# Optimization experiments

Measured on AMD Instinct MI355X. Metric: run time of the kernel, lower is better.

## Reference

```python
import jax, jax.numpy as jnp
import numpy as np

POOL = 7  # cfg.POOLING_SIZE


def roi_align_avg(feat, rois, scale):
    """Legacy RoIAlignAvg: bilinearly sample a (POOL+1)x(POOL+1) grid per RoI
    (crop_and_resize semantics: grid spans roi with divisor G-1), then 2x2
    average-pool with stride 1 -> POOL x POOL output. feat: [B,C,H,W]."""
    B, C, H, W = feat.shape
    G = POOL + 1
    b = rois[:, 0].astype(jnp.int32)                                  # [R]
    x1 = rois[:, 1] * scale
    y1 = rois[:, 2] * scale
    x2 = rois[:, 3] * scale
    y2 = rois[:, 4] * scale
    t = jnp.arange(G, dtype=feat.dtype) / (G - 1)                     # [G]
    ty = jnp.clip(y1[:, None] + (y2 - y1)[:, None] * t, 0.0, H - 1)   # [R,G] rows
    tx = jnp.clip(x1[:, None] + (x2 - x1)[:, None] * t, 0.0, W - 1)   # [R,G] cols
    y0f, x0f = jnp.floor(ty), jnp.floor(tx)
    wy = (ty - y0f)[:, :, None, None]                                 # row frac
    wx = (tx - x0f)[:, None, :, None]                                 # col frac
    y0 = y0f.astype(jnp.int32)
    x0 = x0f.astype(jnp.int32)
    y1i = jnp.minimum(y0 + 1, H - 1)
    x1i = jnp.minimum(x0 + 1, W - 1)

    def g(yi, xi):  # point gather -> [R,G,G,C]
        return feat[b[:, None, None], :, yi[:, :, None], xi[:, None, :]]

    v = ((1 - wy) * ((1 - wx) * g(y0, x0) + wx * g(y0, x1i))
         + wy * ((1 - wx) * g(y1i, x0) + wx * g(y1i, x1i)))           # [R,G,G,C]
    v = jnp.transpose(v, (0, 3, 1, 2))                                # [R,C,G,G]
    # 2x2 avg pool, stride 1 -> [R,C,POOL,POOL]
    return 0.25 * (v[:, :, :-1, :-1] + v[:, :, 1:, :-1]
                   + v[:, :, :-1, 1:] + v[:, :, 1:, 1:])


def reference(p2, p3, p4, p5, rois, im_info):
    """_PyramidRoI_Feat (POOLING_MODE='align'): data-dependent FPN level
    assignment per RoI, per-level RoIAlignAvg, reassembled in original RoI
    order (equivalent to the concat+sort in the torch code)."""
    h = rois[:, 4] - rois[:, 2] + 1.0
    w = rois[:, 3] - rois[:, 1] + 1.0
    lvl = jnp.floor(jnp.log(jnp.sqrt(h * w) / 224.0) / np.float32(np.log(2.0)) + 4.0)
    lvl = jnp.clip(lvl, 2.0, 5.0)                                     # [R]
    im_h = im_info[0, 0]
    out = 0.0
    for l, feat in zip((2, 3, 4, 5), (p2, p3, p4, p5)):
        scale = feat.shape[2] / im_h
        mask = (lvl == l).astype(feat.dtype)[:, None, None, None]
        out = out + mask * roi_align_avg(feat, rois, scale)
    return out  # [R, C, POOL, POOL]


def setup_inputs() -> dict:
    key = jax.random.key(0)
    ks = jax.random.split(key, 6)
    B, C = 1, 256
    IMH = IMW = 1024.0
    R = 2000
    p2 = jax.random.normal(ks[0], (B, C, 256, 256), jnp.float32)
    p3 = jax.random.normal(ks[1], (B, C, 128, 128), jnp.float32)
    p4 = jax.random.normal(ks[2], (B, C, 64, 64), jnp.float32)
    p5 = jax.random.normal(ks[3], (B, C, 32, 32), jnp.float32)
    # log-uniform box sizes so RoIs spread across all 4 pyramid levels
    wh = jnp.exp(jax.random.uniform(ks[4], (R, 2), jnp.float32,
                                    minval=np.log(16.0), maxval=np.log(600.0)))
    xy = jax.random.uniform(ks[5], (R, 2), jnp.float32) * (jnp.array([IMW, IMH]) - wh)
    rois = jnp.concatenate([
        jnp.zeros((R, 1), jnp.float32),            # batch index
        xy[:, 0:1], xy[:, 1:2],                    # x1, y1
        xy[:, 0:1] + wh[:, 0:1] - 1.0,             # x2
        xy[:, 1:2] + wh[:, 1:2] - 1.0,             # y2
    ], axis=1)
    im_info = jnp.array([[IMH, IMW, 1.0]], jnp.float32)
    return {"p2": p2, "p3": p3, "p4": p4, "p5": p5, "rois": rois, "im_info": im_info}
```

## Files before the change

kernel.cpp:

```cpp
#include <hip/hip_runtime.h>
#include <hip/hip_fp16.h>
#include <math.h>

#define POOLSZ 7
#define GRIDG 8
#define CCH  256
#define NBIN 256
#define OPP  (POOLSZ * POOLSZ)
#define MAXPER 8

typedef float  fx4 __attribute__((ext_vector_type(4)));

__device__ __forceinline__ int roi_level(const float* __restrict__ rois, int r) {
    const float x1 = rois[r * 5 + 1];
    const float y1 = rois[r * 5 + 2];
    const float x2 = rois[r * 5 + 3];
    const float y2 = rois[r * 5 + 4];
    const float h = __fadd_rn(__fsub_rn(y2, y1), 1.0f);
    const float w = __fadd_rn(__fsub_rn(x2, x1), 1.0f);
    const float s = __fsqrt_rn(__fmul_rn(h, w));
    const float LOG2 = __uint_as_float(0x3F317218u);
    float lv = floorf(__fadd_rn(__fdiv_rn(logf(__fdiv_rn(s, 224.0f)), LOG2), 4.0f));
    lv = fminf(fmaxf(lv, 2.0f), 5.0f);
    return (int)lv;
}

__global__ __launch_bounds__(256) void prep_kernel(
    const float* __restrict__ p2, const float* __restrict__ p3,
    const float* __restrict__ p4, const float* __restrict__ p5,
    __half* __restrict__ t2, __half* __restrict__ t3,
    __half* __restrict__ t4, __half* __restrict__ t5,
    int HW2, int HW3, int HW4, int HW5,
    const float* __restrict__ rois, const float* __restrict__ im_info,
    int R, int* __restrict__ sorted, int nblkT)
{
    const int t = threadIdx.x;

    if ((int)blockIdx.x == nblkT) {
        __shared__ int cnt[NBIN];
        __shared__ int tmp[NBIN];
        cnt[t] = 0;
        __syncthreads();

        int myR[MAXPER], myBin[MAXPER], mySlot[MAXPER];
        int m = 0;
        const float ih = im_info[0], iw = im_info[1];
        for (int r = t; r < R && m < MAXPER; r += 256) {
            const int lvl = roi_level(rois, r);
            const float cx = 0.5f * (rois[r * 5 + 1] + rois[r * 5 + 3]);
            const float cy = 0.5f * (rois[r * 5 + 2] + rois[r * 5 + 4]);
            const int tx = min(7, max(0, (int)(cx * 8.0f / iw)));
            const int ty = min(7, max(0, (int)(cy * 8.0f / ih)));
            const int bin = (ty * 8 + tx) * 4 + (lvl - 2);
            myR[m] = r; myBin[m] = bin;
            mySlot[m] = atomicAdd(&cnt[bin], 1);
            ++m;
        }
        __syncthreads();

        const int v = cnt[t];
        tmp[t] = v;
        __syncthreads();
        for (int s = 1; s < NBIN; s <<= 1) {
            const int u = (t >= s) ? tmp[t - s] : 0;
            __syncthreads();
            tmp[t] += u;
            __syncthreads();
        }
        cnt[t] = tmp[t] - v;
        __syncthreads();

        for (int i = 0; i < m; ++i)
            sorted[cnt[myBin[i]] + mySlot[i]] = myR[i];
        return;
    }

    const int n2 = (HW2 / 64) * 4, n3 = (HW3 / 64) * 4, n4 = (HW4 / 64) * 4;
    int bid = blockIdx.x;
    const float* src; __half* dst; int HW;
    if (bid < n2)              { src = p2; dst = t2; HW = HW2; }
    else if ((bid -= n2) < n3) { src = p3; dst = t3; HW = HW3; }
    else if ((bid -= n3) < n4) { src = p4; dst = t4; HW = HW4; }
    else { bid -= n4;            src = p5; dst = t5; HW = HW5; }
    const int ptiles = HW / 64;
    const int pt = bid % ptiles, ct = bid / ptiles;
    const int pbase = pt * 64, cbase = ct * 64;

    __shared__ float tile[64][65];

    const int l = t & 15, cr = t >> 4;
#pragma unroll
    for (int p = 0; p < 4; ++p) {
        const int c = p * 16 + cr;
        const fx4* sp = (const fx4*)(src + (size_t)(cbase + c) * HW + pbase + l * 4);
        const fx4 v = __builtin_nontemporal_load(sp);
        tile[c][l * 4 + 0] = v.x;
        tile[c][l * 4 + 1] = v.y;
        tile[c][l * 4 + 2] = v.z;
        tile[c][l * 4 + 3] = v.w;
    }
    __syncthreads();

    const int ch2 = t & 31, pr = t >> 5;
#pragma unroll
    for (int p = 0; p < 8; ++p) {
        const int row = p * 8 + pr;
        const __half2 h = __floats2half2_rn(tile[ch2 * 2][row], tile[ch2 * 2 + 1][row]);
        *(__half2*)(dst + (size_t)(pbase + row) * CCH + cbase + ch2 * 2) = h;
    }
}

__global__ __launch_bounds__(256) void fpn_main_t(
    const __half* __restrict__ t2, const __half* __restrict__ t3,
    const __half* __restrict__ t4, const __half* __restrict__ t5,
    const float* __restrict__ rois, const float* __restrict__ im_info,
    float* __restrict__ out, const int* __restrict__ order,
    int H2, int H3, int H4, int H5, int R)
{
    const int n = blockIdx.x;
    const int q = R / 8, rem = R % 8;
    const int xcd = n % 8, idx = n / 8;
    const int nsw = (xcd < rem ? xcd * (q + 1) : rem * (q + 1) + (xcd - rem) * q) + idx;
    const int r = order ? order[nsw] : nsw;
    const int t = threadIdx.x;

    const float x1 = rois[r * 5 + 1];
    const float y1 = rois[r * 5 + 2];
    const float x2 = rois[r * 5 + 3];
    const float y2 = rois[r * 5 + 4];

    const int lvl = roi_level(rois, r);
    const __half* feat;
    int H;
    switch (lvl) {
        case 2:  feat = t2; H = H2; break;
        case 3:  feat = t3; H = H3; break;
        case 4:  feat = t4; H = H4; break;
        default: feat = t5; H = H5; break;
    }
    const int W = H;

    const float im_h  = im_info[0];
    const float scale = __fdiv_rn((float)H, im_h);
    const float ylo = __fmul_rn(y1, scale), yhi = __fmul_rn(y2, scale);
    const float xlo = __fmul_rn(x1, scale), xhi = __fmul_rn(x2, scale);

    float wy[GRIDG], wx[GRIDG];
    int yoff[GRIDG], dy[GRIDG], xoff[GRIDG], dx[GRIDG];
#pragma unroll
    for (int i = 0; i < GRIDG; ++i) {
        const float tf = __fdiv_rn((float)i, (float)(GRIDG - 1));
        float ty = __fadd_rn(ylo, __fmul_rn(__fsub_rn(yhi, ylo), tf));
        ty = fminf(fmaxf(ty, 0.0f), (float)(H - 1));
        const float y0f = floorf(ty);
        const int   y0  = (int)y0f;
        yoff[i] = y0 * W * CCH;
        dy[i]   = (min(y0 + 1, H - 1) - y0) * W * CCH;
        wy[i]   = __fsub_rn(ty, y0f);

        float tx = __fadd_rn(xlo, __fmul_rn(__fsub_rn(xhi, xlo), tf));
        tx = fminf(fmaxf(tx, 0.0f), (float)(W - 1));
        const float x0f = floorf(tx);
        const int   x0  = (int)x0f;
        xoff[i] = x0 * CCH;
        dx[i]   = (min(x0 + 1, W - 1) - x0) * CCH;
        wx[i]   = __fsub_rn(tx, x0f);
    }

    __shared__ float s_out[CCH * OPP];

    float rowPrev[GRIDG], rowCur[GRIDG];
#pragma unroll
    for (int gy = 0; gy < GRIDG; ++gy) {
        const __half* base = feat + yoff[gy] + t;
        const int dyg = dy[gy];
        const float wyg = wy[gy];
        const float omy = 1.0f - wyg;
#pragma unroll
        for (int gx = 0; gx < GRIDG; ++gx) {
            const __half* qp = base + xoff[gx];
            const int dxg = dx[gx];
            const float v00 = __half2float(qp[0]);
            const float v01 = __half2float(qp[dxg]);
            const float v10 = __half2float(qp[dyg]);
            const float v11 = __half2float(qp[dyg + dxg]);
            const float wxg = wx[gx];
            const float omx = 1.0f - wxg;
            rowCur[gx] = omy * (omx * v00 + wxg * v01) + wyg * (omx * v10 + wxg * v11);
        }
        if (gy > 0) {
            const int py = gy - 1;
#pragma unroll
            for (int px = 0; px < POOLSZ; ++px) {
                s_out[t * OPP + py * POOLSZ + px] =
                    0.25f * (rowPrev[px] + rowPrev[px + 1] + rowCur[px] + rowCur[px + 1]);
            }
        }
#pragma unroll
        for (int gx = 0; gx < GRIDG; ++gx) rowPrev[gx] = rowCur[gx];
    }

    __syncthreads();
    float* obase = out + (size_t)r * (CCH * OPP);
    const float* sp = s_out;
#pragma unroll
    for (int i = 0; i < 12; ++i) {
        const unsigned k4 = (unsigned)(i * 256 + t) * 4u;
        fx4 v;
        v.x = sp[k4 + 0]; v.y = sp[k4 + 1]; v.z = sp[k4 + 2]; v.w = sp[k4 + 3];
        __builtin_nontemporal_store(v, (fx4*)(obase + k4));
    }
    if (t < 64) {
        const unsigned k4 = (unsigned)(12 * 256 + t) * 4u;
        fx4 v;
        v.x = sp[k4 + 0]; v.y = sp[k4 + 1]; v.z = sp[k4 + 2]; v.w = sp[k4 + 3];
        __builtin_nontemporal_store(v, (fx4*)(obase + k4));
    }
}

__global__ __launch_bounds__(256) void fpn_roialign_kernel(
    const float* __restrict__ p2, const float* __restrict__ p3,
    const float* __restrict__ p4, const float* __restrict__ p5,
    const float* __restrict__ rois, const float* __restrict__ im_info,
    float* __restrict__ out, const int* __restrict__ order,
    int H2, int H3, int H4, int H5, int R)
{
    const int n = blockIdx.x;
    const int q = R / 8, rem = R % 8;
    const int xcd = n % 8, idx = n / 8;
    const int nsw = (xcd < rem ? xcd * (q + 1) : rem * (q + 1) + (xcd - rem) * q) + idx;
    const int r = order ? order[nsw] : nsw;

    const float bf = rois[r * 5 + 0];
    const float x1 = rois[r * 5 + 1];
    const float y1 = rois[r * 5 + 2];
    const float x2 = rois[r * 5 + 3];
    const float y2 = rois[r * 5 + 4];

    const int lvl = roi_level(rois, r);
    const float* feat;
    int H;
    switch (lvl) {
        case 2:  feat = p2; H = H2; break;
        case 3:  feat = p3; H = H3; break;
        case 4:  feat = p4; H = H4; break;
        default: feat = p5; H = H5; break;
    }
    const int W = H;
    const int wv  = threadIdx.x >> 6;
    const int lid = threadIdx.x & 63;
    const int gy  = lid >> 3;
    const int gx  = lid & 7;

    const float im_h  = im_info[0];
    const float scale = __fdiv_rn((float)H, im_h);
    const float ylo = __fmul_rn(y1, scale), yhi = __fmul_rn(y2, scale);
    const float xlo = __fmul_rn(x1, scale), xhi = __fmul_rn(x2, scale);
    float ty = __fadd_rn(ylo, __fmul_rn(__fsub_rn(yhi, ylo),
                                        __fdiv_rn((float)gy, (float)(GRIDG - 1))));
    ty = fminf(fmaxf(ty, 0.0f), (float)(H - 1));
    float tx = __fadd_rn(xlo, __fmul_rn(__fsub_rn(xhi, xlo),
                                        __fdiv_rn((float)gx, (float)(GRIDG - 1))));
    tx = fminf(fmaxf(tx, 0.0f), (float)(W - 1));
    const float y0f = floorf(ty), x0f = floorf(tx);
    const int   y0  = (int)y0f,   x0  = (int)x0f;
    const int   y1i = min(y0 + 1, H - 1);
    const int   x1i = min(x0 + 1, W - 1);
    const float wyv = __fsub_rn(ty, y0f);
    const float wxv = __fsub_rn(tx, x0f);
    const float omy = 1.0f - wyv;
    const float omx = 1.0f - wxv;

    const int b = (int)bf;
    const size_t plane = (size_t)H * W;
    const float* fbase = feat + (size_t)(b * CCH + wv * 64) * plane;
    const int o00 = y0  * W + x0;
    const int o01 = y0  * W + x1i;
    const int o10 = y1i * W + x0;
    const int o11 = y1i * W + x1i;

    float* obase = out + (size_t)r * (CCH * OPP) + (size_t)(wv * 64) * OPP;
    const bool wr  = (gy < POOLSZ) && (gx < POOLSZ);
    const int oidx = gy * POOLSZ + gx;

#pragma unroll 4
    for (int k = 0; k < 64; ++k) {
        const float* f = fbase + (size_t)k * plane;
        const float v00 = f[o00];
        const float v01 = f[o01];
        const float v10 = f[o10];
        const float v11 = f[o11];
        const float v = omy * (omx * v00 + wxv * v01) + wyv * (omx * v10 + wxv * v11);
        const float vb  = __shfl_down(v, 8);
        const float vr  = __shfl_down(v, 1);
        const float vbr = __shfl_down(v, 9);
        if (wr) obase[k * OPP + oidx] = 0.25f * (((v + vb) + vr) + vbr);
    }
}

extern "C" void kernel_launch(void* const* d_in, const int* in_sizes, int n_in,
                              void* d_out, int out_size, void* d_ws, size_t ws_size,
                              hipStream_t stream) {
    const float* p2      = (const float*)d_in[0];
    const float* p3      = (const float*)d_in[1];
    const float* p4      = (const float*)d_in[2];
    const float* p5      = (const float*)d_in[3];
    const float* rois    = (const float*)d_in[4];
    const float* im_info = (const float*)d_in[5];
    float* out = (float*)d_out;

    const int R = in_sizes[4] / 5;
    auto dimOf = [](int sz) {
        int hw = sz / CCH;
        return (int)(sqrtf((float)hw) + 0.5f);
    };
    const int H2 = dimOf(in_sizes[0]);
    const int H3 = dimOf(in_sizes[1]);
    const int H4 = dimOf(in_sizes[2]);
    const int H5 = dimOf(in_sizes[3]);
    const size_t HW2 = (size_t)H2 * H2, HW3 = (size_t)H3 * H3;
    const size_t HW4 = (size_t)H4 * H4, HW5 = (size_t)H5 * H5;

    const size_t sortBytes = (size_t)R * sizeof(int);
    const size_t sortPad   = (sortBytes + 255) & ~(size_t)255;
    const size_t transBytes = (HW2 + HW3 + HW4 + HW5) * CCH * sizeof(__half);
    const bool canSort  = (ws_size >= sortBytes) && (R <= 256 * MAXPER);
    const bool canTrans = ws_size >= sortPad + transBytes;

    if (canTrans) {
        int* sorted = canSort ? (int*)d_ws : nullptr;
        __half* t2 = (__half*)((char*)d_ws + sortPad);
        __half* t3 = t2 + HW2 * CCH;
        __half* t4 = t3 + HW3 * CCH;
        __half* t5 = t4 + HW4 * CCH;
        const int nblkT = (int)((HW2 + HW3 + HW4 + HW5) / 64 * 4);
        const int nblk  = nblkT + (canSort ? 1 : 0);
        prep_kernel<<<nblk, 256, 0, stream>>>(
            p2, p3, p4, p5, t2, t3, t4, t5,
            (int)HW2, (int)HW3, (int)HW4, (int)HW5,
            rois, im_info, R, sorted, nblkT);
        fpn_main_t<<<R, 256, 0, stream>>>(
            t2, t3, t4, t5, rois, im_info, out, sorted, H2, H3, H4, H5, R);
    } else {
        fpn_roialign_kernel<<<R, 256, 0, stream>>>(
            p2, p3, p4, p5, rois, im_info, out, nullptr, H2, H3, H4, H5, R);
    }
}
```

Before: 63.63 us.

## Split RoI grid rows across thread halves with half2 channel-pair loads

```diff
diff --git a/kernel.cpp b/kernel.cpp
--- a/kernel.cpp
+++ b/kernel.cpp
@@ -9,7 +9,7 @@
 #define OPP  (POOLSZ * POOLSZ)
 #define MAXPER 8
 
-typedef float  fx4 __attribute__((ext_vector_type(4)));
+typedef float fx4 __attribute__((ext_vector_type(4)));
 
 __device__ __forceinline__ int roi_level(const float* __restrict__ rois, int r) {
     const float x1 = rois[r * 5 + 1];
@@ -123,6 +123,9 @@
     const int nsw = (xcd < rem ? xcd * (q + 1) : rem * (q + 1) + (xcd - rem) * q) + idx;
     const int r = order ? order[nsw] : nsw;
     const int t = threadIdx.x;
+    const int cpair = t & 127;
+    const int grp   = t >> 7;
+    const int c0    = cpair * 2;
 
     const float x1 = rois[r * 5 + 1];
     const float y1 = rois[r * 5 + 2];
@@ -145,55 +148,71 @@
     const float ylo = __fmul_rn(y1, scale), yhi = __fmul_rn(y2, scale);
     const float xlo = __fmul_rn(x1, scale), xhi = __fmul_rn(x2, scale);
 
-    float wy[GRIDG], wx[GRIDG];
-    int yoff[GRIDG], dy[GRIDG], xoff[GRIDG], dx[GRIDG];
+    float wx[GRIDG];
+    int xoff[GRIDG], dxo[GRIDG];
 #pragma unroll
     for (int i = 0; i < GRIDG; ++i) {
         const float tf = __fdiv_rn((float)i, (float)(GRIDG - 1));
+        float tx = __fadd_rn(xlo, __fmul_rn(__fsub_rn(xhi, xlo), tf));
+        tx = fminf(fmaxf(tx, 0.0f), (float)(W - 1));
+        const float x0f = floorf(tx);
+        const int   x0  = (int)x0f;
+        xoff[i] = x0 * CCH;
+        dxo[i]  = (min(x0 + 1, W - 1) - x0) * CCH;
+        wx[i]   = __fsub_rn(tx, x0f);
+    }
+
+    float wyv[5];
+    int yoff[5], dyo[5];
+#pragma unroll
+    for (int i = 0; i < 5; ++i) {
+        const int gy = min(grp * 4 + i, GRIDG - 1);
+        const float tf = __fdiv_rn((float)gy, (float)(GRIDG - 1));
         float ty = __fadd_rn(ylo, __fmul_rn(__fsub_rn(yhi, ylo), tf));
         ty = fminf(fmaxf(ty, 0.0f), (float)(H - 1));
         const float y0f = floorf(ty);
         const int   y0  = (int)y0f;
         yoff[i] = y0 * W * CCH;
-        dy[i]   = (min(y0 + 1, H - 1) - y0) * W * CCH;
-        wy[i]   = __fsub_rn(ty, y0f);
-
-        float tx = __fadd_rn(xlo, __fmul_rn(__fsub_rn(xhi, xlo), tf));
-        tx = fminf(fmaxf(tx, 0.0f), (float)(W - 1));
-        const float x0f = floorf(tx);
-        const int   x0  = (int)x0f;
-        xoff[i] = x0 * CCH;
-        dx[i]   = (min(x0 + 1, W - 1) - x0) * CCH;
-        wx[i]   = __fsub_rn(tx, x0f);
+        dyo[i]  = (min(y0 + 1, H - 1) - y0) * W * CCH;
+        wyv[i]  = __fsub_rn(ty, y0f);
     }
 
     __shared__ float s_out[CCH * OPP];
 
-    float rowPrev[GRIDG], rowCur[GRIDG];
-#pragma unroll
-    for (int gy = 0; gy < GRIDG; ++gy) {
-        const __half* base = feat + yoff[gy] + t;
-        const int dyg = dy[gy];
-        const float wyg = wy[gy];
+    const __half* fb = feat + c0;
+    float2 rowPrev[GRIDG], rowCur[GRIDG];
+#pragma unroll
+    for (int i = 0; i < 5; ++i) {
+        if (grp == 1 && i == 4) break;
+        const __half* base = fb + yoff[i];
+        const int dyg = dyo[i];
+        const float wyg = wyv[i];
         const float omy = 1.0f - wyg;
 #pragma unroll
         for (int gx = 0; gx < GRIDG; ++gx) {
             const __half* qp = base + xoff[gx];
-            const int dxg = dx[gx];
-            const float v00 = __half2float(qp[0]);
-            const float v01 = __half2float(qp[dxg]);
-            const float v10 = __half2float(qp[dyg]);
-            const float v11 = __half2float(qp[dyg + dxg]);
+            const int dxg = dxo[gx];
+            const float2 v00 = __half22float2(*(const __half2*)(qp));
+            const float2 v01 = __half22float2(*(const __half2*)(qp + dxg));
+            const float2 v10 = __half22float2(*(const __half2*)(qp + dyg));
+            const float2 v11 = __half22float2(*(const __half2*)(qp + dyg + dxg));
             const float wxg = wx[gx];
             const float omx = 1.0f - wxg;
-            rowCur[gx] = omy * (omx * v00 + wxg * v01) + wyg * (omx * v10 + wxg * v11);
+            rowCur[gx].x = omy * (omx * v00.x + wxg * v01.x)
+                         + wyg * (omx * v10.x + wxg * v11.x);
+            rowCur[gx].y = omy * (omx * v00.y + wxg * v01.y)
+                         + wyg * (omx * v10.y + wxg * v11.y);
         }
-        if (gy > 0) {
-            const int py = gy - 1;
+        if (i > 0) {
+            const int py = grp * 4 + i - 1;
 #pragma unroll
             for (int px = 0; px < POOLSZ; ++px) {
-                s_out[t * OPP + py * POOLSZ + px] =
-                    0.25f * (rowPrev[px] + rowPrev[px + 1] + rowCur[px] + rowCur[px + 1]);
+                const float pvx = 0.25f * (rowPrev[px].x + rowPrev[px + 1].x
+                                           + rowCur[px].x + rowCur[px + 1].x);
+                const float pvy = 0.25f * (rowPrev[px].y + rowPrev[px + 1].y
+                                           + rowCur[px].y + rowCur[px + 1].y);
+                s_out[c0 * OPP + py * POOLSZ + px] = pvx;
+                s_out[(c0 + 1) * OPP + py * POOLSZ + px] = pvy;
             }
         }
 #pragma unroll
@@ -222,14 +241,10 @@
     const float* __restrict__ p2, const float* __restrict__ p3,
     const float* __restrict__ p4, const float* __restrict__ p5,
     const float* __restrict__ rois, const float* __restrict__ im_info,
-    float* __restrict__ out, const int* __restrict__ order,
+    float* __restrict__ out,
     int H2, int H3, int H4, int H5, int R)
 {
-    const int n = blockIdx.x;
-    const int q = R / 8, rem = R % 8;
-    const int xcd = n % 8, idx = n / 8;
-    const int nsw = (xcd < rem ? xcd * (q + 1) : rem * (q + 1) + (xcd - rem) * q) + idx;
-    const int r = order ? order[nsw] : nsw;
+    const int r = blockIdx.x;
 
     const float bf = rois[r * 5 + 0];
     const float x1 = rois[r * 5 + 1];
@@ -343,6 +358,6 @@
             t2, t3, t4, t5, rois, im_info, out, sorted, H2, H3, H4, H5, R);
     } else {
         fpn_roialign_kernel<<<R, 256, 0, stream>>>(
-            p2, p3, p4, p5, rois, im_info, out, nullptr, H2, H3, H4, H5, R);
-    }
-}
+            p2, p3, p4, p5, rois, im_info, out, H2, H3, H4, H5, R);
+    }
+}
```

Measured after the change: 62.07 us. 2.5% less time.
